# Performance work log

Measured on AMD Instinct MI355X. Metric: run time of the kernel, lower is better.

The kernel has to match this reference:

```python
import jax, jax.numpy as jnp
import numpy as np

N = 100000       # nodes
E = 1600000      # edges (avg degree 16)
F_IN, H, C = 128, 128, 47


def setup_inputs() -> dict:
    key = jax.random.key(0)
    ks = jax.random.split(key, 12)
    def lin(k, fan_in, fan_out):
        return (jax.random.normal(k, (fan_in, fan_out), dtype=jnp.float32)
                / np.float32(np.sqrt(fan_in)))
    return {
        "x": jax.random.normal(ks[0], (N, F_IN), dtype=jnp.float32),
        "src": jax.random.randint(ks[1], (E,), 0, N, dtype=jnp.int32),
        "dst": jax.random.randint(ks[2], (E,), 0, N, dtype=jnp.int32),
        "w_self0": lin(ks[3], F_IN, H),
        "w_neigh0": lin(ks[4], F_IN, H),
        "b0": jnp.zeros((H,), jnp.float32),
        "w_self1": lin(ks[5], H, H),
        "w_neigh1": lin(ks[6], H, H),
        "b1": jnp.zeros((H,), jnp.float32),
        "w_self2": lin(ks[7], H, C),
        "w_neigh2": lin(ks[8], H, C),
        "b2": jnp.zeros((C,), jnp.float32),
    }


def _sage_layer(h, src, dst, w_self, w_neigh, b):
    # mean-aggregate neighbor features: gather h[src], scatter-add to dst
    agg = jax.ops.segment_sum(h[src], dst, num_segments=N)        # [N, d]
    deg = jax.ops.segment_sum(jnp.ones((src.shape[0], 1), h.dtype), dst,
                              num_segments=N)                     # [N, 1]
    mean = agg / jnp.maximum(deg, 1.0)
    # DGL SAGEConv('mean'): fc_self(h_dst) + fc_neigh(mean) + bias
    return h @ w_self + mean @ w_neigh + b


def reference(x, src, dst,
              w_self0, w_neigh0, b0,
              w_self1, w_neigh1, b1,
              w_self2, w_neigh2, b2):
    h = _sage_layer(x, src, dst, w_self0, w_neigh0, b0)
    h = jax.nn.relu(h)  # dropout is identity in eval mode
    h = _sage_layer(h, src, dst, w_self1, w_neigh1, b1)
    h = jax.nn.relu(h)
    h = _sage_layer(h, src, dst, w_self2, w_neigh2, b2)
    return h
```

## Files before the change

kernel.cpp:

```cpp
#include <hip/hip_runtime.h>

typedef unsigned int u32;
typedef unsigned short u16;
typedef __attribute__((ext_vector_type(8))) short short8;
typedef __attribute__((ext_vector_type(4))) float f32x4;

__device__ __forceinline__ u16 f2bf(float f) {
    u32 u = __float_as_uint(f);
    u32 r = (u + 0x7fffu + ((u >> 16) & 1u)) >> 16;
    return (u16)r;
}
__device__ __forceinline__ float bf2f(u32 lo16) { return __uint_as_float(lo16 << 16); }

__device__ __forceinline__ void acc_u4p(float2* a, uint4 v) {
    u32 w[4] = {v.x, v.y, v.z, v.w};
#pragma unroll
    for (int i = 0; i < 4; i++) {
        float2 t;
        t.x = __uint_as_float(w[i] << 16);
        t.y = __uint_as_float(w[i] & 0xffff0000u);
        a[i].x += t.x;
        a[i].y += t.y;
    }
}


__global__ __launch_bounds__(256) void prep_w_all(const float* __restrict__ ws0, const float* __restrict__ wn0, u16* __restrict__ wt0,
                                                  const float* __restrict__ ws1, const float* __restrict__ wn1, u16* __restrict__ wt1,
                                                  const float* __restrict__ ws2, const float* __restrict__ wn2, u16* __restrict__ wt2) {
    int bid = blockIdx.x;
    const float *ws, *wn;
    u16* wt;
    int dout, HW, local;
    if (bid < 128)      { ws = ws0; wn = wn0; wt = wt0; dout = 128; HW = 128; local = bid; }
    else if (bid < 256) { ws = ws1; wn = wn1; wt = wt1; dout = 128; HW = 128; local = bid - 128; }
    else                { ws = ws2; wn = wn2; wt = wt2; dout = 47;  HW = 64;  local = bid - 256; }
    int idx = local * 256 + threadIdx.x;
    int n = idx >> 7, k = idx & 127;
    float v = 0.f;
    if (n < HW) { if (n < dout) v = ws[k * dout + n]; }
    else { int nn = n - HW; if (nn < dout) v = wn[k * dout + nn]; }
    wt[idx] = f2bf(v);
}


__global__ __launch_bounds__(256) void hist256(const int* __restrict__ dst,
                                               int* __restrict__ bcnt, int E) {
    __shared__ int bins[256];
    bins[threadIdx.x] = 0;
    __syncthreads();
    int gid = blockIdx.x * 256 + threadIdx.x;
    int stride = gridDim.x * 256;
    const int4* d4 = (const int4*)dst;
    int n4 = E >> 2;
    for (int k = gid; k < n4; k += stride) {
        int4 v = d4[k];
        atomicAdd(&bins[v.x >> 9], 1);
        atomicAdd(&bins[v.y >> 9], 1);
        atomicAdd(&bins[v.z >> 9], 1);
        atomicAdd(&bins[v.w >> 9], 1);
    }
    for (int k = (n4 << 2) + gid; k < E; k += stride)
        atomicAdd(&bins[dst[k] >> 9], 1);
    __syncthreads();
    int b = bins[threadIdx.x];
    if (b) atomicAdd(&bcnt[threadIdx.x], b);
}

__global__ __launch_bounds__(256) void scan256(const int* __restrict__ bcnt,
                                               int* __restrict__ boff,
                                               int* __restrict__ cursor) {
    __shared__ int sm[256];
    int t = threadIdx.x;
    int v = bcnt[t];
    sm[t] = v;
    __syncthreads();
    for (int off = 1; off < 256; off <<= 1) {
        int u = (t >= off) ? sm[t - off] : 0;
        __syncthreads();
        sm[t] += u;
        __syncthreads();
    }
    int excl = sm[t] - v;
    boff[t] = excl;
    cursor[t] = excl;
    if (t == 255) boff[256] = sm[255];
}

#define TILE 4096
__global__ __launch_bounds__(512) void bucket_scatter(const int* __restrict__ src,
                                                      const int* __restrict__ dst,
                                                      int* __restrict__ cursor,
                                                      uint2* __restrict__ pairs, int E) {
    __shared__ uint2 sp[TILE];
    __shared__ int s_cnt[256], s_off[256], s_gpos[256], s_cnt2[256];
    const int tid = threadIdx.x;
    const int base = blockIdx.x * TILE;
    const int tn = min(TILE, E - base);
    if (tid < 256) { s_cnt[tid] = 0; s_cnt2[tid] = 0; }
    __syncthreads();
    int d[8], s[8];
#pragma unroll
    for (int j = 0; j < 8; j++) {
        int k = tid + j * 512;
        if (k < tn) {
            d[j] = dst[base + k];
            s[j] = src[base + k];
            atomicAdd(&s_cnt[d[j] >> 9], 1);
        } else d[j] = -1;
    }
    __syncthreads();
    if (tid < 256) s_off[tid] = s_cnt[tid];
    __syncthreads();
    for (int off = 1; off < 256; off <<= 1) {
        int v = 0;
        if (tid < 256 && tid >= off) v = s_off[tid - off];
        __syncthreads();
        if (tid < 256) s_off[tid] += v;
        __syncthreads();
    }
    if (tid < 256 && s_cnt[tid] > 0) s_gpos[tid] = atomicAdd(&cursor[tid], s_cnt[tid]);
    __syncthreads();
#pragma unroll
    for (int j = 0; j < 8; j++) {
        if (d[j] >= 0) {
            int b = d[j] >> 9;
            int p = atomicAdd(&s_cnt2[b], 1);
            sp[s_off[b] - s_cnt[b] + p] = make_uint2((u32)d[j], (u32)s[j]);
        }
    }
    __syncthreads();
    for (int k = tid; k < tn; k += 512) {
        uint2 pr = sp[k];
        int b = (int)(pr.x >> 9);
        pairs[s_gpos[b] + (k - (s_off[b] - s_cnt[b]))] = pr;
    }
}

#define LDSCAP 12288
__global__ __launch_bounds__(512) void build_csr2(const uint2* __restrict__ pairs,
                                                  const int* __restrict__ boff,
                                                  int* __restrict__ rowptr,
                                                  float* __restrict__ invd,
                                                  int* __restrict__ cols, int Nn, int E) {
    __shared__ int s_pack[LDSCAP];
    __shared__ int s_cols[LDSCAP];
    __shared__ int s_cnt[512];
    __shared__ int s_off[512];
    __shared__ int s_cnt2[512];
    const int tid = threadIdx.x;
    const int d0 = blockIdx.x * 512;
    const int nd = min(512, Nn - d0);
    const int base = boff[blockIdx.x];
    const int n = boff[blockIdx.x + 1] - base;
    const bool fit = (n <= LDSCAP);
    s_cnt[tid] = 0; s_cnt2[tid] = 0;
    __syncthreads();
    for (int k = tid; k < n; k += 512) {
        uint2 pr = pairs[base + k];
        int dl = (int)pr.x - d0;
        atomicAdd(&s_cnt[dl], 1);
        if (fit) s_pack[k] = (dl << 17) | (int)pr.y;
    }
    __syncthreads();
    int v = s_cnt[tid];
    s_off[tid] = v;
    __syncthreads();
    for (int off = 1; off < 512; off <<= 1) {
        int u = (tid >= off) ? s_off[tid - off] : 0;
        __syncthreads();
        s_off[tid] += u;
        __syncthreads();
    }
    int excl = s_off[tid] - v;
    if (tid < nd) {
        rowptr[d0 + tid] = base + excl;
        invd[d0 + tid] = 1.0f / (float)max(v, 1);
    }
    if (blockIdx.x == 0 && tid == 0) rowptr[Nn] = E;
    s_off[tid] = excl;
    __syncthreads();
    if (fit) {
        for (int k = tid; k < n; k += 512) {
            int pk = s_pack[k];
            int dl = pk >> 17;
            int p = atomicAdd(&s_cnt2[dl], 1);
            s_cols[s_off[dl] + p] = pk & 0x1ffff;
        }
        __syncthreads();
        for (int k = tid; k < n; k += 512) cols[base + k] = s_cols[k];
    } else {
        for (int k = tid; k < n; k += 512) {
            uint2 pr = pairs[base + k];
            int dl = (int)pr.x - d0;
            int p = atomicAdd(&s_cnt2[dl], 1);
            cols[base + s_off[dl] + p] = (int)pr.y;
        }
    }
}

#define KDIM 128
#define KP 136

template <int NCOLS, bool AF32>
__global__ __launch_bounds__(256) void gemm_bf16(const void* __restrict__ Ap,
                                                 const u16* __restrict__ Bt,
                                                 u16* __restrict__ C, int M) {
    __shared__ u16 As[64 * KP];
    __shared__ u16 Bs[128 * KP];
    const int row0 = blockIdx.x * 64;
    const int col0 = blockIdx.y * 128;
    const int tid = threadIdx.x;

#pragma unroll
    for (int i = 0; i < 4; i++) {
        int idx = tid + i * 256;
        int r = idx >> 4, c = idx & 15;
        uint4 v = make_uint4(0, 0, 0, 0);
        if (row0 + r < M) {
            if (AF32) {
                const float* Af = (const float*)Ap;
                const float4* rowp = (const float4*)(Af + (size_t)(row0 + r) * KDIM);
                float4 f0 = rowp[2 * c];
                float4 f1 = rowp[2 * c + 1];
                v.x = (u32)f2bf(f0.x) | ((u32)f2bf(f0.y) << 16);
                v.y = (u32)f2bf(f0.z) | ((u32)f2bf(f0.w) << 16);
                v.z = (u32)f2bf(f1.x) | ((u32)f2bf(f1.y) << 16);
                v.w = (u32)f2bf(f1.z) | ((u32)f2bf(f1.w) << 16);
            } else {
                const u16* Ab = (const u16*)Ap;
                v = ((const uint4*)(Ab + (size_t)(row0 + r) * KDIM))[c];
            }
        }
        ((uint4*)(As + r * KP))[c] = v;
    }
#pragma unroll
    for (int i = 0; i < 8; i++) {
        int idx = tid + i * 256;
        int r = idx >> 4, c = idx & 15;
        uint4 v = ((const uint4*)(Bt + (size_t)(col0 + r) * KDIM))[c];
        ((uint4*)(Bs + r * KP))[c] = v;
    }
    __syncthreads();

    const int lane = tid & 63, wave = tid >> 6;
    const int quad = lane >> 4, l16 = lane & 15;
    const int wcol = wave * 32;

    f32x4 acc[4][2];
#pragma unroll
    for (int mt = 0; mt < 4; mt++)
#pragma unroll
        for (int nt = 0; nt < 2; nt++) acc[mt][nt] = (f32x4){0.f, 0.f, 0.f, 0.f};

#pragma unroll
    for (int kc = 0; kc < 4; kc++) {
        short8 a[4], b[2];
#pragma unroll
        for (int mt = 0; mt < 4; mt++)
            a[mt] = *(const short8*)(As + (size_t)(mt * 16 + l16) * KP + kc * 32 + quad * 8);
#pragma unroll
        for (int nt = 0; nt < 2; nt++)
            b[nt] = *(const short8*)(Bs + (size_t)(wcol + nt * 16 + l16) * KP + kc * 32 + quad * 8);
#pragma unroll
        for (int mt = 0; mt < 4; mt++)
#pragma unroll
            for (int nt = 0; nt < 2; nt++)
                acc[mt][nt] = __builtin_amdgcn_mfma_f32_16x16x32_bf16(a[mt], b[nt], acc[mt][nt], 0, 0, 0);
    }

    __syncthreads();
#pragma unroll
    for (int mt = 0; mt < 4; mt++)
#pragma unroll
        for (int i = 0; i < 4; i++) {
            int rl = mt * 16 + quad * 4 + i;
#pragma unroll
            for (int nt = 0; nt < 2; nt++)
                As[rl * KP + wcol + nt * 16 + l16] = f2bf(acc[mt][nt][i]);
        }
    __syncthreads();
#pragma unroll
    for (int it = 0; it < 4; it++) {
        int idx = tid + it * 256;
        int r = idx >> 4, c8 = idx & 15;
        if (row0 + r < M)
            *(uint4*)(C + (size_t)(row0 + r) * NCOLS + col0 + c8 * 8) =
                *(const uint4*)(As + r * KP + c8 * 8);
    }
}

template <bool RELU>
__global__ __launch_bounds__(256) void agg128_k(const u16* __restrict__ out2,
                                                const int* __restrict__ rowptr,
                                                const int* __restrict__ cols,
                                                const float* __restrict__ invd,
                                                const float* __restrict__ bias,
                                                u16* __restrict__ outp, int Mn) {
    int wave = threadIdx.x >> 6, lane = threadIdx.x & 63;
    int node = blockIdx.x * 4 + wave;
    if (node >= Mn) return;
    int sub = lane >> 4, l16 = lane & 15;
    const u16* tb = out2 + 128 + 8 * l16;
    int beg = rowptr[node], end = rowptr[node + 1];
    float2 a[4];
#pragma unroll
    for (int i = 0; i < 4; i++) a[i] = make_float2(0.f, 0.f);
    int e = beg + sub;
    while (e < end) {
        int s0 = cols[e];
        int s1 = (e + 4  < end) ? cols[e + 4]  : Mn;
        int s2 = (e + 8  < end) ? cols[e + 8]  : Mn;
        int s3 = (e + 12 < end) ? cols[e + 12] : Mn;
        uint4 v0 = *(const uint4*)(tb + (size_t)s0 * 256);
        uint4 v1 = *(const uint4*)(tb + (size_t)s1 * 256);
        uint4 v2 = *(const uint4*)(tb + (size_t)s2 * 256);
        uint4 v3 = *(const uint4*)(tb + (size_t)s3 * 256);
        acc_u4p(a, v0); acc_u4p(a, v1); acc_u4p(a, v2); acc_u4p(a, v3);
        e += 16;
    }
    float af[8] = {a[0].x, a[0].y, a[1].x, a[1].y, a[2].x, a[2].y, a[3].x, a[3].y};
#pragma unroll
    for (int j = 0; j < 8; j++) {
        af[j] += __shfl_xor(af[j], 16); af[j] += __shfl_xor(af[j], 32);
    }
    if (sub == 0) {
        float id = invd[node];
        uint4 sv = *(const uint4*)(out2 + (size_t)node * 256 + 8 * l16);
        float4 b0 = *(const float4*)(bias + 8 * l16);
        float4 b1 = *(const float4*)(bias + 8 * l16 + 4);
        float o0 = bf2f(sv.x & 0xffffu) + af[0] * id + b0.x;
        float o1 = bf2f(sv.x >> 16)     + af[1] * id + b0.y;
        float o2 = bf2f(sv.y & 0xffffu) + af[2] * id + b0.z;
        float o3 = bf2f(sv.y >> 16)     + af[3] * id + b0.w;
        float o4 = bf2f(sv.z & 0xffffu) + af[4] * id + b1.x;
        float o5 = bf2f(sv.z >> 16)     + af[5] * id + b1.y;
        float o6 = bf2f(sv.w & 0xffffu) + af[6] * id + b1.z;
        float o7 = bf2f(sv.w >> 16)     + af[7] * id + b1.w;
        if (RELU) {
            o0 = fmaxf(o0, 0.f); o1 = fmaxf(o1, 0.f); o2 = fmaxf(o2, 0.f); o3 = fmaxf(o3, 0.f);
            o4 = fmaxf(o4, 0.f); o5 = fmaxf(o5, 0.f); o6 = fmaxf(o6, 0.f); o7 = fmaxf(o7, 0.f);
        }
        uint4 w;
        w.x = (u32)f2bf(o0) | ((u32)f2bf(o1) << 16);
        w.y = (u32)f2bf(o2) | ((u32)f2bf(o3) << 16);
        w.z = (u32)f2bf(o4) | ((u32)f2bf(o5) << 16);
        w.w = (u32)f2bf(o6) | ((u32)f2bf(o7) << 16);
        *(uint4*)(outp + (size_t)node * 128 + 8 * l16) = w;
    }
}

__global__ __launch_bounds__(256) void agg_out8_k(const u16* __restrict__ out2,
                                                  const int* __restrict__ rowptr,
                                                  const int* __restrict__ cols,
                                                  const float* __restrict__ invd,
                                                  const float* __restrict__ bias,
                                                  float* __restrict__ outp, int Mn) {
    int wave = threadIdx.x >> 6, lane = threadIdx.x & 63;
    int node = blockIdx.x * 4 + wave;
    if (node >= Mn) return;
    int e8 = lane >> 3, l8 = lane & 7;
    const u16* tb = out2 + 64 + 8 * l8;
    int beg = rowptr[node], end = rowptr[node + 1];
    float2 a[4];
#pragma unroll
    for (int i = 0; i < 4; i++) a[i] = make_float2(0.f, 0.f);
    int e = beg + e8;
    while (e < end) {
        int s0 = cols[e];
        int s1 = (e + 8  < end) ? cols[e + 8]  : Mn;
        int s2 = (e + 16 < end) ? cols[e + 16] : Mn;
        int s3 = (e + 24 < end) ? cols[e + 24] : Mn;
        uint4 v0 = *(const uint4*)(tb + (size_t)s0 * 128);
        uint4 v1 = *(const uint4*)(tb + (size_t)s1 * 128);
        uint4 v2 = *(const uint4*)(tb + (size_t)s2 * 128);
        uint4 v3 = *(const uint4*)(tb + (size_t)s3 * 128);
        acc_u4p(a, v0); acc_u4p(a, v1); acc_u4p(a, v2); acc_u4p(a, v3);
        e += 32;
    }
    float af[8] = {a[0].x, a[0].y, a[1].x, a[1].y, a[2].x, a[2].y, a[3].x, a[3].y};
#pragma unroll
    for (int j = 0; j < 8; j++) {
        af[j] += __shfl_xor(af[j], 8); af[j] += __shfl_xor(af[j], 16); af[j] += __shfl_xor(af[j], 32);
    }
    if (e8 == 0) {
        float id = invd[node];
        uint4 sv = *(const uint4*)(out2 + (size_t)node * 128 + 8 * l8);
        u32 sw[4] = {sv.x, sv.y, sv.z, sv.w};
        float* orow = outp + (size_t)node * 47;
#pragma unroll
        for (int j = 0; j < 8; j++) {
            int c = 8 * l8 + j;
            if (c < 47) {
                float s = bf2f((j & 1) ? (sw[j >> 1] >> 16) : (sw[j >> 1] & 0xffffu));
                orow[c] = s + af[j] * id + bias[c];
            }
        }
    }
}


extern "C" void kernel_launch(void* const* d_in, const int* in_sizes, int n_in,
                              void* d_out, int out_size, void* d_ws, size_t ws_size,
                              hipStream_t stream) {
    const float* x   = (const float*)d_in[0];
    const int*   src = (const int*)d_in[1];
    const int*   dst = (const int*)d_in[2];
    const float* ws0 = (const float*)d_in[3];
    const float* wn0 = (const float*)d_in[4];
    const float* b0  = (const float*)d_in[5];
    const float* ws1 = (const float*)d_in[6];
    const float* wn1 = (const float*)d_in[7];
    const float* b1  = (const float*)d_in[8];
    const float* ws2 = (const float*)d_in[9];
    const float* wn2 = (const float*)d_in[10];
    const float* b2  = (const float*)d_in[11];

    const int Nn = in_sizes[0] / 128;
    const int E  = in_sizes[1];

    char* p = (char*)d_ws;
    auto alloc = [&](size_t bytes) -> void* {
        void* r = (void*)p;
        p += (bytes + 255) & ~(size_t)255;
        return r;
    };
    u16*   bufA   = (u16*)alloc((size_t)Nn * 128 * 2);
    u16*   out2   = (u16*)alloc(((size_t)Nn * 256 + 256) * 2);
    u16*   wt0    = (u16*)alloc(256 * 128 * 2);
    u16*   wt1    = (u16*)alloc(256 * 128 * 2);
    u16*   wt2    = (u16*)alloc(128 * 128 * 2);
    int*   rowptr = (int*)alloc((size_t)(Nn + 1) * 4);
    float* invd   = (float*)alloc((size_t)Nn * 4);
    int*   cols   = (int*)alloc((size_t)(E + 32) * 4);
    int*   bcnt   = (int*)alloc(256 * 4);
    int*   boff   = (int*)alloc(257 * 4);
    int*   cursor = (int*)alloc(256 * 4);
    uint2* pairs  = (uint2*)out2;

    hipMemsetAsync(bcnt, 0, 256 * 4, stream);
    hipMemsetAsync(out2 + (size_t)Nn * 256, 0, 512, stream);

    prep_w_all<<<320, 256, 0, stream>>>(ws0, wn0, wt0, ws1, wn1, wt1, ws2, wn2, wt2);

    hist256<<<512, 256, 0, stream>>>(dst, bcnt, E);
    scan256<<<1, 256, 0, stream>>>(bcnt, boff, cursor);

    bucket_scatter<<<(E + TILE - 1) / TILE, 512, 0, stream>>>(src, dst, cursor, pairs, E);
    build_csr2<<<(Nn + 511) / 512, 512, 0, stream>>>(pairs, boff, rowptr, invd, cols, Nn, E);

    dim3 ggrid((Nn + 63) / 64, 2);
    dim3 ggrid1((Nn + 63) / 64, 1);
    const int aggGrid = (Nn + 3) / 4;
    gemm_bf16<256, true><<<ggrid, 256, 0, stream>>>(x, wt0, out2, Nn);
    agg128_k<true><<<aggGrid, 256, 0, stream>>>(out2, rowptr, cols, invd, b0, bufA, Nn);
    gemm_bf16<256, false><<<ggrid, 256, 0, stream>>>(bufA, wt1, out2, Nn);
    agg128_k<true><<<aggGrid, 256, 0, stream>>>(out2, rowptr, cols, invd, b1, bufA, Nn);
    gemm_bf16<128, false><<<ggrid1, 256, 0, stream>>>(bufA, wt2, out2, Nn);
    hipMemsetAsync(out2 + (size_t)Nn * 128, 0, 256, stream);
    agg_out8_k<<<aggGrid, 256, 0, stream>>>(out2, rowptr, cols, invd, b2, (float*)d_out, Nn);
}
```

Baseline: 393.8 us.

## Replace CSR adjacency with fixed 32-slot ELL layout plus overflow pool

The row-pointer CSR build is replaced by a padded ELL table: each destination node gets 32 neighbour slots filled with a sentinel row index, and edges beyond 32 go to a global overflow pool. The aggregation kernels then issue a fixed, fully unrolled set of gathers per node with no rowptr loads, loop bounds or scan in the build kernel. Small follow-up kernels recompute the rare overflowing nodes by scanning the pool. In exchange every node pays for 32 slots, so index traffic roughly doubles and sentinel gathers are added. Edges beyond the pool capacity would be silently dropped.

Result: slower. 410.5 us (+4.2%).

```diff
diff --git a/kernel.cpp b/kernel.cpp
--- a/kernel.cpp
+++ b/kernel.cpp
@@ -5,6 +5,8 @@
 typedef __attribute__((ext_vector_type(8))) short short8;
 typedef __attribute__((ext_vector_type(4))) float f32x4;
 
+#define POOLCAP 65536
+
 __device__ __forceinline__ u16 f2bf(float f) {
     u32 u = __float_as_uint(f);
     u32 r = (u + 0x7fffu + ((u >> 16) & 1u)) >> 16;
@@ -16,11 +18,8 @@
     u32 w[4] = {v.x, v.y, v.z, v.w};
 #pragma unroll
     for (int i = 0; i < 4; i++) {
-        float2 t;
-        t.x = __uint_as_float(w[i] << 16);
-        t.y = __uint_as_float(w[i] & 0xffff0000u);
-        a[i].x += t.x;
-        a[i].y += t.y;
+        a[i].x += __uint_as_float(w[i] << 16);
+        a[i].y += __uint_as_float(w[i] & 0xffff0000u);
     }
 }
 
@@ -138,65 +137,73 @@
 }
 
 #define LDSCAP 12288
-__global__ __launch_bounds__(512) void build_csr2(const uint2* __restrict__ pairs,
+__global__ __launch_bounds__(512) void build_csr3(const uint2* __restrict__ pairs,
                                                   const int* __restrict__ boff,
-                                                  int* __restrict__ rowptr,
                                                   float* __restrict__ invd,
-                                                  int* __restrict__ cols, int Nn, int E) {
+                                                  int* __restrict__ colsF,
+                                                  uint2* __restrict__ pool,
+                                                  int* __restrict__ gcnt,
+                                                  int Nn) {
     __shared__ int s_pack[LDSCAP];
-    __shared__ int s_cols[LDSCAP];
+    __shared__ int s_fix[512 * 32];
     __shared__ int s_cnt[512];
-    __shared__ int s_off[512];
-    __shared__ int s_cnt2[512];
     const int tid = threadIdx.x;
     const int d0 = blockIdx.x * 512;
     const int nd = min(512, Nn - d0);
     const int base = boff[blockIdx.x];
     const int n = boff[blockIdx.x + 1] - base;
     const bool fit = (n <= LDSCAP);
-    s_cnt[tid] = 0; s_cnt2[tid] = 0;
-    __syncthreads();
-    for (int k = tid; k < n; k += 512) {
-        uint2 pr = pairs[base + k];
-        int dl = (int)pr.x - d0;
-        atomicAdd(&s_cnt[dl], 1);
-        if (fit) s_pack[k] = (dl << 17) | (int)pr.y;
-    }
-    __syncthreads();
-    int v = s_cnt[tid];
-    s_off[tid] = v;
-    __syncthreads();
-    for (int off = 1; off < 512; off <<= 1) {
-        int u = (tid >= off) ? s_off[tid - off] : 0;
-        __syncthreads();
-        s_off[tid] += u;
-        __syncthreads();
-    }
-    int excl = s_off[tid] - v;
-    if (tid < nd) {
-        rowptr[d0 + tid] = base + excl;
-        invd[d0 + tid] = 1.0f / (float)max(v, 1);
-    }
-    if (blockIdx.x == 0 && tid == 0) rowptr[Nn] = E;
-    s_off[tid] = excl;
+    s_cnt[tid] = 0;
+    {
+        int4 sv4 = make_int4(Nn, Nn, Nn, Nn);
+        int4* p4 = (int4*)s_fix;
+        for (int k = tid; k < 512 * 32 / 4; k += 512) p4[k] = sv4;
+    }
+    __syncthreads();
+    if (fit) {
+        for (int k = tid; k < n; k += 512) {
+            uint2 pr = pairs[base + k];
+            int dl = (int)pr.x - d0;
+            atomicAdd(&s_cnt[dl], 1);
+            s_pack[k] = (dl << 17) | (int)pr.y;
+        }
+    } else {
+        for (int k = tid; k < n; k += 512) {
+            uint2 pr = pairs[base + k];
+            atomicAdd(&s_cnt[(int)pr.x - d0], 1);
+        }
+    }
+    __syncthreads();
+    if (tid < nd) invd[d0 + tid] = 1.0f / (float)max(s_cnt[tid], 1);
+    s_cnt[tid] = 0;
     __syncthreads();
     if (fit) {
         for (int k = tid; k < n; k += 512) {
             int pk = s_pack[k];
-            int dl = pk >> 17;
-            int p = atomicAdd(&s_cnt2[dl], 1);
-            s_cols[s_off[dl] + p] = pk & 0x1ffff;
-        }
-        __syncthreads();
-        for (int k = tid; k < n; k += 512) cols[base + k] = s_cols[k];
+            int dl = pk >> 17, sc = pk & 0x1ffff;
+            int p = atomicAdd(&s_cnt[dl], 1);
+            if (p < 32) s_fix[dl * 32 + p] = sc;
+            else {
+                int q = atomicAdd(gcnt, 1);
+                if (q < POOLCAP) pool[q] = make_uint2((u32)(d0 + dl), (u32)sc);
+            }
+        }
     } else {
         for (int k = tid; k < n; k += 512) {
             uint2 pr = pairs[base + k];
             int dl = (int)pr.x - d0;
-            int p = atomicAdd(&s_cnt2[dl], 1);
-            cols[base + s_off[dl] + p] = (int)pr.y;
-        }
-    }
+            int p = atomicAdd(&s_cnt[dl], 1);
+            if (p < 32) s_fix[dl * 32 + p] = (int)pr.y;
+            else {
+                int q = atomicAdd(gcnt, 1);
+                if (q < POOLCAP) pool[q] = make_uint2((u32)(d0 + dl), pr.y);
+            }
+        }
+    }
+    __syncthreads();
+    int4* dst4 = (int4*)(colsF + (size_t)d0 * 32);
+    const int4* s4 = (const int4*)s_fix;
+    for (int k = tid; k < 512 * 32 / 4; k += 512) dst4[k] = s4[k];
 }
 
 #define KDIM 128
@@ -291,44 +298,42 @@
 }
 
 template <bool RELU>
-__global__ __launch_bounds__(256) void agg128_k(const u16* __restrict__ out2,
-                                                const int* __restrict__ rowptr,
-                                                const int* __restrict__ cols,
-                                                const float* __restrict__ invd,
-                                                const float* __restrict__ bias,
-                                                u16* __restrict__ outp, int Mn) {
+__global__ __launch_bounds__(256) void agg128f_k(const u16* __restrict__ out2,
+                                                 const int* __restrict__ colsF,
+                                                 const float* __restrict__ invd,
+                                                 const float* __restrict__ bias,
+                                                 u16* __restrict__ outp, int Mn) {
     int wave = threadIdx.x >> 6, lane = threadIdx.x & 63;
     int node = blockIdx.x * 4 + wave;
     if (node >= Mn) return;
     int sub = lane >> 4, l16 = lane & 15;
     const u16* tb = out2 + 128 + 8 * l16;
-    int beg = rowptr[node], end = rowptr[node + 1];
+    const int* cp = colsF + node * 32 + sub;
+    int s0 = cp[0],  s1 = cp[4],  s2 = cp[8],  s3 = cp[12];
+    int s4 = cp[16], s5 = cp[20], s6 = cp[24], s7 = cp[28];
+    float id = invd[node];
+    uint4 sv = *(const uint4*)(out2 + (size_t)node * 256 + 8 * l16);
+    float4 b0 = *(const float4*)(bias + 8 * l16);
+    float4 b1 = *(const float4*)(bias + 8 * l16 + 4);
+    uint4 v0 = *(const uint4*)(tb + (size_t)s0 * 256);
+    uint4 v1 = *(const uint4*)(tb + (size_t)s1 * 256);
+    uint4 v2 = *(const uint4*)(tb + (size_t)s2 * 256);
+    uint4 v3 = *(const uint4*)(tb + (size_t)s3 * 256);
+    uint4 v4 = *(const uint4*)(tb + (size_t)s4 * 256);
+    uint4 v5 = *(const uint4*)(tb + (size_t)s5 * 256);
+    uint4 v6 = *(const uint4*)(tb + (size_t)s6 * 256);
+    uint4 v7 = *(const uint4*)(tb + (size_t)s7 * 256);
     float2 a[4];
 #pragma unroll
     for (int i = 0; i < 4; i++) a[i] = make_float2(0.f, 0.f);
-    int e = beg + sub;
-    while (e < end) {
-        int s0 = cols[e];
-        int s1 = (e + 4  < end) ? cols[e + 4]  : Mn;
-        int s2 = (e + 8  < end) ? cols[e + 8]  : Mn;
-        int s3 = (e + 12 < end) ? cols[e + 12] : Mn;
-        uint4 v0 = *(const uint4*)(tb + (size_t)s0 * 256);
-        uint4 v1 = *(const uint4*)(tb + (size_t)s1 * 256);
-        uint4 v2 = *(const uint4*)(tb + (size_t)s2 * 256);
-        uint4 v3 = *(const uint4*)(tb + (size_t)s3 * 256);
-        acc_u4p(a, v0); acc_u4p(a, v1); acc_u4p(a, v2); acc_u4p(a, v3);
-        e += 16;
-    }
+    acc_u4p(a, v0); acc_u4p(a, v1); acc_u4p(a, v2); acc_u4p(a, v3);
+    acc_u4p(a, v4); acc_u4p(a, v5); acc_u4p(a, v6); acc_u4p(a, v7);
     float af[8] = {a[0].x, a[0].y, a[1].x, a[1].y, a[2].x, a[2].y, a[3].x, a[3].y};
 #pragma unroll
     for (int j = 0; j < 8; j++) {
         af[j] += __shfl_xor(af[j], 16); af[j] += __shfl_xor(af[j], 32);
     }
     if (sub == 0) {
-        float id = invd[node];
-        uint4 sv = *(const uint4*)(out2 + (size_t)node * 256 + 8 * l16);
-        float4 b0 = *(const float4*)(bias + 8 * l16);
-        float4 b1 = *(const float4*)(bias + 8 * l16 + 4);
         float o0 = bf2f(sv.x & 0xffffu) + af[0] * id + b0.x;
         float o1 = bf2f(sv.x >> 16)     + af[1] * id + b0.y;
         float o2 = bf2f(sv.y & 0xffffu) + af[2] * id + b0.z;
@@ -350,42 +355,34 @@
     }
 }
 
-__global__ __launch_bounds__(256) void agg_out8_k(const u16* __restrict__ out2,
-                                                  const int* __restrict__ rowptr,
-                                                  const int* __restrict__ cols,
-                                                  const float* __restrict__ invd,
-                                                  const float* __restrict__ bias,
-                                                  float* __restrict__ outp, int Mn) {
+__global__ __launch_bounds__(256) void agg_out8f_k(const u16* __restrict__ out2,
+                                                   const int* __restrict__ colsF,
+                                                   const float* __restrict__ invd,
+                                                   const float* __restrict__ bias,
+                                                   float* __restrict__ outp, int Mn) {
     int wave = threadIdx.x >> 6, lane = threadIdx.x & 63;
     int node = blockIdx.x * 4 + wave;
     if (node >= Mn) return;
     int e8 = lane >> 3, l8 = lane & 7;
     const u16* tb = out2 + 64 + 8 * l8;
-    int beg = rowptr[node], end = rowptr[node + 1];
+    const int* cp = colsF + node * 32 + e8;
+    int s0 = cp[0], s1 = cp[8], s2 = cp[16], s3 = cp[24];
+    float id = invd[node];
+    uint4 sv = *(const uint4*)(out2 + (size_t)node * 128 + 8 * l8);
+    uint4 v0 = *(const uint4*)(tb + (size_t)s0 * 128);
+    uint4 v1 = *(const uint4*)(tb + (size_t)s1 * 128);
+    uint4 v2 = *(const uint4*)(tb + (size_t)s2 * 128);
+    uint4 v3 = *(const uint4*)(tb + (size_t)s3 * 128);
     float2 a[4];
 #pragma unroll
     for (int i = 0; i < 4; i++) a[i] = make_float2(0.f, 0.f);
-    int e = beg + e8;
-    while (e < end) {
-        int s0 = cols[e];
-        int s1 = (e + 8  < end) ? cols[e + 8]  : Mn;
-        int s2 = (e + 16 < end) ? cols[e + 16] : Mn;
-        int s3 = (e + 24 < end) ? cols[e + 24] : Mn;
-        uint4 v0 = *(const uint4*)(tb + (size_t)s0 * 128);
-        uint4 v1 = *(const uint4*)(tb + (size_t)s1 * 128);
-        uint4 v2 = *(const uint4*)(tb + (size_t)s2 * 128);
-        uint4 v3 = *(const uint4*)(tb + (size_t)s3 * 128);
-        acc_u4p(a, v0); acc_u4p(a, v1); acc_u4p(a, v2); acc_u4p(a, v3);
-        e += 32;
-    }
+    acc_u4p(a, v0); acc_u4p(a, v1); acc_u4p(a, v2); acc_u4p(a, v3);
     float af[8] = {a[0].x, a[0].y, a[1].x, a[1].y, a[2].x, a[2].y, a[3].x, a[3].y};
 #pragma unroll
     for (int j = 0; j < 8; j++) {
         af[j] += __shfl_xor(af[j], 8); af[j] += __shfl_xor(af[j], 16); af[j] += __shfl_xor(af[j], 32);
     }
     if (e8 == 0) {
-        float id = invd[node];
-        uint4 sv = *(const uint4*)(out2 + (size_t)node * 128 + 8 * l8);
         u32 sw[4] = {sv.x, sv.y, sv.z, sv.w};
         float* orow = outp + (size_t)node * 47;
 #pragma unroll
@@ -394,6 +391,101 @@
             if (c < 47) {
                 float s = bf2f((j & 1) ? (sw[j >> 1] >> 16) : (sw[j >> 1] & 0xffffu));
                 orow[c] = s + af[j] * id + bias[c];
+            }
+        }
+    }
+}
+
+template <int MODE>
+__global__ __launch_bounds__(256) void oflow_k(const uint2* __restrict__ pool,
+                                               const int* __restrict__ gcnt,
+                                               const int* __restrict__ colsF,
+                                               const u16* __restrict__ out2,
+                                               const float* __restrict__ invd,
+                                               const float* __restrict__ bias,
+                                               void* __restrict__ outp, int Mn) {
+    int cnt = min(*gcnt, POOLCAP);
+    int wid = blockIdx.x * 4 + (threadIdx.x >> 6);
+    int lane = threadIdx.x & 63;
+    int nw = gridDim.x * 4;
+    for (int i = wid; i < cnt; i += nw) {
+        int node = (int)pool[i].x;
+        float id = invd[node];
+        if (MODE == 0) {
+            int sub = lane >> 4, l16 = lane & 15;
+            const u16* tb = out2 + 128 + 8 * l16;
+            float2 a[4];
+#pragma unroll
+            for (int q = 0; q < 4; q++) a[q] = make_float2(0.f, 0.f);
+#pragma unroll
+            for (int k = 0; k < 8; k++) {
+                int s = colsF[node * 32 + sub + 4 * k];
+                acc_u4p(a, *(const uint4*)(tb + (size_t)s * 256));
+            }
+            for (int j = 0; j < cnt; j++) {
+                uint2 pe = pool[j];
+                if ((int)pe.x == node && sub == (j & 3))
+                    acc_u4p(a, *(const uint4*)(tb + (size_t)pe.y * 256));
+            }
+            float af[8] = {a[0].x, a[0].y, a[1].x, a[1].y, a[2].x, a[2].y, a[3].x, a[3].y};
+#pragma unroll
+            for (int j = 0; j < 8; j++) {
+                af[j] += __shfl_xor(af[j], 16); af[j] += __shfl_xor(af[j], 32);
+            }
+            if (sub == 0) {
+                uint4 sv = *(const uint4*)(out2 + (size_t)node * 256 + 8 * l16);
+                float4 b0 = *(const float4*)(bias + 8 * l16);
+                float4 b1 = *(const float4*)(bias + 8 * l16 + 4);
+                float o0 = bf2f(sv.x & 0xffffu) + af[0] * id + b0.x;
+                float o1 = bf2f(sv.x >> 16)     + af[1] * id + b0.y;
+                float o2 = bf2f(sv.y & 0xffffu) + af[2] * id + b0.z;
+                float o3 = bf2f(sv.y >> 16)     + af[3] * id + b0.w;
+                float o4 = bf2f(sv.z & 0xffffu) + af[4] * id + b1.x;
+                float o5 = bf2f(sv.z >> 16)     + af[5] * id + b1.y;
+                float o6 = bf2f(sv.w & 0xffffu) + af[6] * id + b1.z;
+                float o7 = bf2f(sv.w >> 16)     + af[7] * id + b1.w;
+                o0 = fmaxf(o0, 0.f); o1 = fmaxf(o1, 0.f); o2 = fmaxf(o2, 0.f); o3 = fmaxf(o3, 0.f);
+                o4 = fmaxf(o4, 0.f); o5 = fmaxf(o5, 0.f); o6 = fmaxf(o6, 0.f); o7 = fmaxf(o7, 0.f);
+                uint4 w;
+                w.x = (u32)f2bf(o0) | ((u32)f2bf(o1) << 16);
+                w.y = (u32)f2bf(o2) | ((u32)f2bf(o3) << 16);
+                w.z = (u32)f2bf(o4) | ((u32)f2bf(o5) << 16);
+                w.w = (u32)f2bf(o6) | ((u32)f2bf(o7) << 16);
+                *(uint4*)((u16*)outp + (size_t)node * 128 + 8 * l16) = w;
+            }
+        } else {
+            int e8 = lane >> 3, l8 = lane & 7;
+            const u16* tb = out2 + 64 + 8 * l8;
+            float2 a[4];
+#pragma unroll
+            for (int q = 0; q < 4; q++) a[q] = make_float2(0.f, 0.f);
+#pragma unroll
+            for (int k = 0; k < 4; k++) {
+                int s = colsF[node * 32 + e8 + 8 * k];
+                acc_u4p(a, *(const uint4*)(tb + (size_t)s * 128));
+            }
+            for (int j = 0; j < cnt; j++) {
+                uint2 pe = pool[j];
+                if ((int)pe.x == node && e8 == (j & 7))
+                    acc_u4p(a, *(const uint4*)(tb + (size_t)pe.y * 128));
+            }
+            float af[8] = {a[0].x, a[0].y, a[1].x, a[1].y, a[2].x, a[2].y, a[3].x, a[3].y};
+#pragma unroll
+            for (int j = 0; j < 8; j++) {
+                af[j] += __shfl_xor(af[j], 8); af[j] += __shfl_xor(af[j], 16); af[j] += __shfl_xor(af[j], 32);
+            }
+            if (e8 == 0) {
+                uint4 sv = *(const uint4*)(out2 + (size_t)node * 128 + 8 * l8);
+                u32 sw[4] = {sv.x, sv.y, sv.z, sv.w};
+                float* orow = (float*)outp + (size_t)node * 47;
+#pragma unroll
+                for (int j = 0; j < 8; j++) {
+                    int c = 8 * l8 + j;
+                    if (c < 47) {
+                        float s = bf2f((j & 1) ? (sw[j >> 1] >> 16) : (sw[j >> 1] & 0xffffu));
+                        orow[c] = s + af[j] * id + bias[c];
+                    }
+                }
             }
         }
     }
@@ -418,6 +510,8 @@
 
     const int Nn = in_sizes[0] / 128;
     const int E  = in_sizes[1];
+    const int nBuckets = (Nn + 511) / 512;
+    const int NnPad = nBuckets * 512;
 
     char* p = (char*)d_ws;
     auto alloc = [&](size_t bytes) -> void* {
@@ -430,15 +524,17 @@
     u16*   wt0    = (u16*)alloc(256 * 128 * 2);
     u16*   wt1    = (u16*)alloc(256 * 128 * 2);
     u16*   wt2    = (u16*)alloc(128 * 128 * 2);
-    int*   rowptr = (int*)alloc((size_t)(Nn + 1) * 4);
     float* invd   = (float*)alloc((size_t)Nn * 4);
-    int*   cols   = (int*)alloc((size_t)(E + 32) * 4);
+    int*   colsF  = (int*)alloc((size_t)NnPad * 32 * 4);
+    uint2* pool   = (uint2*)alloc((size_t)POOLCAP * 8);
+    int*   gcnt   = (int*)alloc(256);
     int*   bcnt   = (int*)alloc(256 * 4);
     int*   boff   = (int*)alloc(257 * 4);
     int*   cursor = (int*)alloc(256 * 4);
     uint2* pairs  = (uint2*)out2;
 
     hipMemsetAsync(bcnt, 0, 256 * 4, stream);
+    hipMemsetAsync(gcnt, 0, 4, stream);
     hipMemsetAsync(out2 + (size_t)Nn * 256, 0, 512, stream);
 
     prep_w_all<<<320, 256, 0, stream>>>(ws0, wn0, wt0, ws1, wn1, wt1, ws2, wn2, wt2);
@@ -447,16 +543,19 @@
     scan256<<<1, 256, 0, stream>>>(bcnt, boff, cursor);
 
     bucket_scatter<<<(E + TILE - 1) / TILE, 512, 0, stream>>>(src, dst, cursor, pairs, E);
-    build_csr2<<<(Nn + 511) / 512, 512, 0, stream>>>(pairs, boff, rowptr, invd, cols, Nn, E);
+    build_csr3<<<nBuckets, 512, 0, stream>>>(pairs, boff, invd, colsF, pool, gcnt, Nn);
 
     dim3 ggrid((Nn + 63) / 64, 2);
     dim3 ggrid1((Nn + 63) / 64, 1);
     const int aggGrid = (Nn + 3) / 4;
     gemm_bf16<256, true><<<ggrid, 256, 0, stream>>>(x, wt0, out2, Nn);
-    agg128_k<true><<<aggGrid, 256, 0, stream>>>(out2, rowptr, cols, invd, b0, bufA, Nn);
+    agg128f_k<true><<<aggGrid, 256, 0, stream>>>(out2, colsF, invd, b0, bufA, Nn);
+    oflow_k<0><<<8, 256, 0, stream>>>(pool, gcnt, colsF, out2, invd, b0, bufA, Nn);
     gemm_bf16<256, false><<<ggrid, 256, 0, stream>>>(bufA, wt1, out2, Nn);
-    agg128_k<true><<<aggGrid, 256, 0, stream>>>(out2, rowptr, cols, invd, b1, bufA, Nn);
+    agg128f_k<true><<<aggGrid, 256, 0, stream>>>(out2, colsF, invd, b1, bufA, Nn);
+    oflow_k<0><<<8, 256, 0, stream>>>(pool, gcnt, colsF, out2, invd, b1, bufA, Nn);
     gemm_bf16<128, false><<<ggrid1, 256, 0, stream>>>(bufA, wt2, out2, Nn);
     hipMemsetAsync(out2 + (size_t)Nn * 128, 0, 256, stream);
-    agg_out8_k<<<aggGrid, 256, 0, stream>>>(out2, rowptr, cols, invd, b2, (float*)d_out, Nn);
-}
+    agg_out8f_k<<<aggGrid, 256, 0, stream>>>(out2, colsF, invd, b2, (float*)d_out, Nn);
+    oflow_k<1><<<8, 256, 0, stream>>>(pool, gcnt, colsF, out2, invd, b2, d_out, Nn);
+}
```
